# Kernel tuning notes

Hardware: AMD Instinct MI355X
Metric: run time of the kernel (lower is better)

## Reference

```python
import jax, jax.numpy as jnp
import numpy as np

B, IN_E, IN_I, D = 4096, 4096, 4096, 2048
IN_BR = 8192
BS = IN_BR // D  # block size = 4
K_E, K_I = 50, 1
E_TO_I = 50.0
BN_EPS = 1e-5


def setup_inputs() -> dict:
    key = jax.random.key(0)
    ks = jax.random.split(key, 8)
    # fan-in uniform init like nn.Linear (kaiming-uniform bound ~ 1/sqrt(in))
    def linw(k, out_f, in_f):
        b = 1.0 / np.sqrt(in_f)
        return jax.random.uniform(k, (out_f, in_f), jnp.float32, -b, b)
    return {
        "excitatory_input": jax.random.normal(ks[0], (B, IN_E), jnp.float32),
        "inhibitory_input": jax.random.normal(ks[1], (B, IN_I), jnp.float32),
        "dendrite_branch_outputs": jax.random.uniform(ks[2], (B, IN_BR), jnp.float32),
        "w_exc": linw(ks[3], D, IN_E),
        "w_inh": linw(ks[4], D, IN_I),
        "w_block": linw(ks[5], D, IN_BR),
        "bn_gamma": jnp.ones((D,), jnp.float32),
        "bn_beta": jnp.zeros((D,), jnp.float32),
    }


def _topk_linear(x, w, k):
    # keep the k largest weights per output row, zero the rest, then matmul
    idx = jax.lax.top_k(w, k)[1]                          # [D, k]
    mask = jnp.zeros_like(w).at[jnp.arange(w.shape[0])[:, None], idx].set(1.0)
    return x @ (w * mask).T                               # [B, D]


def _block_linear(x, w):
    # block-diagonal mask: row c uses columns [c*BS, (c+1)*BS)
    out_f = w.shape[0]
    wb = w.reshape(out_f, out_f, BS)[jnp.arange(out_f), jnp.arange(out_f)]  # [D, BS]
    xb = x.reshape(x.shape[0], out_f, BS)                                   # [B, D, BS]
    return jnp.einsum('bds,ds->bd', xb, wb)


def reference(excitatory_input, inhibitory_input, dendrite_branch_outputs,
              w_exc, w_inh, w_block, bn_gamma, bn_beta):
    dendrite_excitation = _topk_linear(excitatory_input, w_exc, K_E)
    dendrite_inhibition = _topk_linear(inhibitory_input, w_inh, K_I)
    dendrite_depolarization = _block_linear(dendrite_branch_outputs, w_block)
    total_excitatory = dendrite_excitation + dendrite_depolarization
    # neuron_type == 'excitatory'
    act = total_excitatory - E_TO_I * dendrite_inhibition
    # BatchNorm1d, training mode: batch stats, biased variance
    mean = jnp.mean(act, axis=0)
    var = jnp.var(act, axis=0)
    act = (act - mean) * jax.lax.rsqrt(var + BN_EPS) * bn_gamma + bn_beta
    return jax.nn.sigmoid(act)
```

## Files before the change

### kernel.cpp

```cpp
#include <hip/hip_runtime.h>
#include <hip/hip_fp16.h>

#define B_     4096
#define INE_   4096
#define INBR_  8192
#define D_     2048
#define KE_    50
#define KPAD_  52
#define CAP_   512
#define NSL_   4

__device__ __forceinline__ unsigned packh2(float a, float b) {
  __half2 h = __floats2half2_rn(a, b);
  return __builtin_bit_cast(unsigned, h);
}
__device__ __forceinline__ float2 unpackh2(unsigned u) {
  __half2 h = __builtin_bit_cast(__half2, u);
  return __half22float2(h);
}

__device__ void topk_body(const float* __restrict__ W, int row, int k, int kpad,
                          float hi, float t0, float vscale,
                          uint4* __restrict__ muT,
                          unsigned* __restrict__ out_off, float* __restrict__ out_val)
{
  const int t = threadIdx.x;
  const float* wr = W + (size_t)row * INE_;

  __shared__ float cval[CAP_];
  __shared__ int   ccol[CAP_];
  __shared__ int   scnt;
  __shared__ int   red[4];

  float thr = t0;
  int M = 0;
  for (int attempt = 0; attempt < 8; ++attempt) {
    int local = 0;
    #pragma unroll
    for (int j = 0; j < 4; ++j) {
      float4 w4 = *reinterpret_cast<const float4*>(wr + 4 * (t + 256 * j));
      local += (w4.x > thr) + (w4.y > thr) + (w4.z > thr) + (w4.w > thr);
    }
    #pragma unroll
    for (int off = 32; off > 0; off >>= 1) local += __shfl_down(local, off);
    if ((t & 63) == 0) red[t >> 6] = local;
    __syncthreads();
    M = red[0] + red[1] + red[2] + red[3];
    __syncthreads();
    if (M >= k && M <= CAP_) break;
    if (M < k) thr = hi - (hi - thr) * 4.0f;
    else       thr = hi - (hi - thr) * 0.5f;
  }

  if (t == 0) scnt = 0;
  __syncthreads();
  #pragma unroll
  for (int j = 0; j < 4; ++j) {
    int cbase = 4 * (t + 256 * j);
    float4 w4 = *reinterpret_cast<const float4*>(wr + cbase);
    float wv[4] = {w4.x, w4.y, w4.z, w4.w};
    #pragma unroll
    for (int q = 0; q < 4; ++q) {
      if (wv[q] > thr) {
        int pp = atomicAdd(&scnt, 1);
        if (pp < CAP_) { cval[pp] = wv[q]; ccol[pp] = cbase + q; }
      }
    }
  }
  __syncthreads();
  M = scnt < CAP_ ? scnt : CAP_;

  for (int i = t; i < M; i += 256) {
    float wi = cval[i]; int ci = ccol[i];
    int rank = 0;
    for (int m = 0; m < M; ++m) {
      float wm = cval[m]; int cm = ccol[m];
      rank += (wm > wi || (wm == wi && cm < ci)) ? 1 : 0;
    }
    if (rank < k) {
      unsigned c = (unsigned)ci;
      if (kpad == 1) {
        out_off[row] = c;
        out_val[row] = wi * vscale;
      } else {
        unsigned off = ((c >> 2) << 3) | ((c & 3u) << 13);
        char* rec = (char*)muT + ((size_t)(rank >> 2) * D_ + row) * 16;
        reinterpret_cast<unsigned short*>(rec)[rank & 3] = (unsigned short)off;
        reinterpret_cast<__half*>(rec)[4 + (rank & 3)] =
            __float2half_rn(wi * vscale);
      }
    }
  }
  if (kpad > 1 && t < kpad - k) {
    int slot = k + t;
    char* rec = (char*)muT + ((size_t)(slot >> 2) * D_ + row) * 16;
    reinterpret_cast<unsigned short*>(rec)[slot & 3] = 0;
    reinterpret_cast<__half*>(rec)[4 + (slot & 3)] = __float2half_rn(0.0f);
  }
}

__global__ __launch_bounds__(256) void prep_kernel(
    const float* __restrict__ wexc, const float* __restrict__ winh,
    const float* __restrict__ wblk,
    uint4* __restrict__ muT,
    unsigned* __restrict__ so_inh, float* __restrict__ vi_inh,
    float* __restrict__ wdiag)
{
  const int bid = blockIdx.x;
  const float hi = 0.015625f;
  if (bid < 2048) {
    topk_body(wexc, bid, KE_, KPAD_, hi, hi * (1.0f - 200.0f / 4096.0f), 1.0f,
              muT, nullptr, nullptr);
  } else if (bid < 4096) {
    topk_body(winh, bid - 2048, 1, 1, hi, hi * (1.0f - 48.0f / 4096.0f), -50.0f,
              nullptr, so_inh, vi_inh);
  } else {
    const int t = threadIdx.x;
    #pragma unroll
    for (int j = 0; j < 8; ++j) {
      int d = t + 256 * j;
      float4 w = *reinterpret_cast<const float4*>(wblk + (size_t)d * (INBR_ + 4));
      reinterpret_cast<float4*>(wdiag)[d] = w;
    }
  }
}

__device__ __forceinline__ uint2 ld8(const char* ldsb, unsigned off) {
  return *reinterpret_cast<const uint2*>(ldsb + off);
}

#define FMA4(R, G, WV) do {                                                \
    float2 f0 = unpackh2((G).x), f1 = unpackh2((G).y);                     \
    acc[R][0] = fmaf(f0.x, (WV), acc[R][0]);                               \
    acc[R][1] = fmaf(f0.y, (WV), acc[R][1]);                               \
    acc[R][2] = fmaf(f1.x, (WV), acc[R][2]);                               \
    acc[R][3] = fmaf(f1.y, (WV), acc[R][3]);                               \
  } while (0)

__global__ __launch_bounds__(512, 4) void fused_ei(
    const float* __restrict__ xe, const float* __restrict__ xi,
    const float* __restrict__ xbr, const float* __restrict__ wdiag,
    const uint4* __restrict__ muT,
    const unsigned* __restrict__ so_inh, const float* __restrict__ vi_inh,
    __half* __restrict__ act_h, float* __restrict__ sums_p,
    float* __restrict__ sumsq_p)
{
  __shared__ unsigned xs[8192];
  const int t  = threadIdx.x;
  const int b0 = blockIdx.x * 4;
  const int p  = t & 1;
  const int Q  = t >> 1;

  float acc[4][4];
  #pragma unroll
  for (int r = 0; r < 4; ++r)
    #pragma unroll
    for (int b = 0; b < 4; ++b) acc[r][b] = 0.0f;

  const char* ldsb = reinterpret_cast<const char*>(xs);

  {
    const float* r0p = xe + (size_t)(b0 + 2 * p)     * INE_;
    const float* r1p = xe + (size_t)(b0 + 2 * p + 1) * INE_;
    #pragma unroll
    for (int m = 0; m < 4; ++m) {
      int c0 = 4 * Q + 1024 * m;
      float4 fa = *reinterpret_cast<const float4*>(r0p + c0);
      float4 fb = *reinterpret_cast<const float4*>(r1p + c0);
      int wb = 2 * (Q + 256 * m) + p;
      xs[wb]        = packh2(fa.x, fb.x);
      xs[wb + 2048] = packh2(fa.y, fb.y);
      xs[wb + 4096] = packh2(fa.z, fb.z);
      xs[wb + 6144] = packh2(fa.w, fb.w);
    }
  }

  unsigned ci[4]; float viv[4];
  #pragma unroll
  for (int r = 0; r < 4; ++r) {
    ci[r]  = so_inh[t + 512 * r];
    viv[r] = vi_inh[t + 512 * r];
  }
  float xg0[4], xg1[4], xg2[4], xg3[4];
  #pragma unroll
  for (int b = 0; b < 4; ++b) {
    const float* xrow = xi + (size_t)(b0 + b) * INE_;
    xg0[b] = xrow[ci[0]];
    xg1[b] = xrow[ci[1]];
    xg2[b] = xrow[ci[2]];
    xg3[b] = xrow[ci[3]];
  }
  __syncthreads();

  for (int ii = 0; ii < KPAD_ / 4; ++ii) {
    uint4 m[4];
    #pragma unroll
    for (int r = 0; r < 4; ++r) m[r] = muT[ii * D_ + t + 512 * r];
    #pragma unroll
    for (int half = 0; half < 2; ++half) {
      uint2 g[2][4];
      #pragma unroll
      for (int rr = 0; rr < 2; ++rr) {
        const int r = 2 * half + rr;
        g[rr][0] = ld8(ldsb, m[r].x & 0xFFFFu);
        g[rr][1] = ld8(ldsb, m[r].x >> 16);
        g[rr][2] = ld8(ldsb, m[r].y & 0xFFFFu);
        g[rr][3] = ld8(ldsb, m[r].y >> 16);
      }
      #pragma unroll
      for (int rr = 0; rr < 2; ++rr) {
        const int r = 2 * half + rr;
        float2 vA = unpackh2(m[r].z);
        float2 vB = unpackh2(m[r].w);
        FMA4(r, g[rr][0], vA.x);
        FMA4(r, g[rr][1], vA.y);
        FMA4(r, g[rr][2], vB.x);
        FMA4(r, g[rr][3], vB.y);
      }
    }
  }

  #pragma unroll
  for (int b = 0; b < 4; ++b) {
    acc[0][b] = fmaf(xg0[b], viv[0], acc[0][b]);
    acc[1][b] = fmaf(xg1[b], viv[1], acc[1][b]);
    acc[2][b] = fmaf(xg2[b], viv[2], acc[2][b]);
    acc[3][b] = fmaf(xg3[b], viv[3], acc[3][b]);
  }

  #pragma unroll
  for (int r = 0; r < 4; ++r) {
    const int d = t + 512 * r;
    float4 wb4 = reinterpret_cast<const float4*>(wdiag)[d];
    #pragma unroll
    for (int b = 0; b < 4; ++b) {
      float4 xb4 = *reinterpret_cast<const float4*>(
          xbr + (size_t)(b0 + b) * INBR_ + 4 * d);
      acc[r][b] += xb4.x * wb4.x + xb4.y * wb4.y + xb4.z * wb4.z + xb4.w * wb4.w;
    }
  }

  const int slice = blockIdx.x & (NSL_ - 1);
  #pragma unroll
  for (int r = 0; r < 4; ++r) {
    const int d = t + 512 * r;
    float s = 0.0f, s2 = 0.0f;
    #pragma unroll
    for (int b = 0; b < 4; ++b) {
      float a = acc[r][b];
      act_h[(size_t)(b0 + b) * D_ + d] = __float2half_rn(a);
      s += a;
      s2 = fmaf(a, a, s2);
    }
    atomicAdd(&sums_p[slice * D_ + d], s);
    atomicAdd(&sumsq_p[slice * D_ + d], s2);
  }
}

__global__ __launch_bounds__(256) void tail_kernel(
    const __half* __restrict__ act_h, float* __restrict__ out,
    const float* __restrict__ sums_p, const float* __restrict__ sumsq_p,
    const float* __restrict__ gamma, const float* __restrict__ beta)
{
  __shared__ float scsh[2 * D_];
  const int tid = threadIdx.x;
  #pragma unroll
  for (int j = 0; j < 8; ++j) {
    int d = tid + 256 * j;
    float s = 0.0f, s2 = 0.0f;
    #pragma unroll
    for (int sl = 0; sl < NSL_; ++sl) {
      s  += sums_p[sl * D_ + d];
      s2 += sumsq_p[sl * D_ + d];
    }
    float mean = s  * (1.0f / B_);
    float var  = s2 * (1.0f / B_) - mean * mean;
    float rstd = rsqrtf(var + 1e-5f);
    float sc   = gamma[d] * rstd;
    scsh[2 * d]     = sc;
    scsh[2 * d + 1] = fmaf(-mean, sc, beta[d]);
  }
  __syncthreads();

  const int r0 = blockIdx.x * 8;
  for (int rr = 0; rr < 8; ++rr) {
    const uint2* ap = reinterpret_cast<const uint2*>(act_h + (size_t)(r0 + rr) * D_);
    float4*      op = reinterpret_cast<float4*>(out + (size_t)(r0 + rr) * D_);
    #pragma unroll
    for (int i2 = 0; i2 < 2; ++i2) {
      int i = tid + 256 * i2;
      uint2 aw = ap[i];
      float2 f0 = unpackh2(aw.x);
      float2 f1 = unpackh2(aw.y);
      const float4* sp = reinterpret_cast<const float4*>(scsh + 8 * i);
      float4 s0 = sp[0];
      float4 s1 = sp[1];
      float z0 = fmaf(f0.x, s0.x, s0.y);
      float z1 = fmaf(f0.y, s0.z, s0.w);
      float z2 = fmaf(f1.x, s1.x, s1.y);
      float z3 = fmaf(f1.y, s1.z, s1.w);
      float4 o;
      o.x = 1.0f / (1.0f + __expf(-z0));
      o.y = 1.0f / (1.0f + __expf(-z1));
      o.z = 1.0f / (1.0f + __expf(-z2));
      o.w = 1.0f / (1.0f + __expf(-z3));
      op[i] = o;
    }
  }
}

extern "C" void kernel_launch(void* const* d_in, const int* in_sizes, int n_in,
                              void* d_out, int out_size, void* d_ws, size_t ws_size,
                              hipStream_t stream) {
  const float* xe    = (const float*)d_in[0];
  const float* xi    = (const float*)d_in[1];
  const float* xbr   = (const float*)d_in[2];
  const float* wexc  = (const float*)d_in[3];
  const float* winh  = (const float*)d_in[4];
  const float* wblk  = (const float*)d_in[5];
  const float* gamma = (const float*)d_in[6];
  const float* beta  = (const float*)d_in[7];
  float* out = (float*)d_out;

  char* ws = (char*)d_ws;
  uint4*    muT     = (uint4*)   (ws + 0);
  unsigned* so_inh  = (unsigned*)(ws + 425984);
  float*    vi_inh  = (float*)   (ws + 434176);
  float*    wdiag   = (float*)   (ws + 442368);
  float*    sums_p  = (float*)   (ws + 475136);
  float*    sumsq_p = (float*)   (ws + 507904);
  __half*   act_h   = (__half*)  (ws + 1048576);

  hipMemsetAsync(sums_p, 0, 2 * NSL_ * D_ * sizeof(float), stream);

  prep_kernel<<<dim3(4097), dim3(256), 0, stream>>>(
      wexc, winh, wblk, muT, so_inh, vi_inh, wdiag);
  fused_ei<<<dim3(B_ / 4), dim3(512), 0, stream>>>(
      xe, xi, xbr, wdiag, muT, so_inh, vi_inh, act_h, sums_p, sumsq_p);
  tail_kernel<<<dim3(512), dim3(256), 0, stream>>>(
      act_h, out, sums_p, sumsq_p, gamma, beta);
}
```

Before: 124.6 us.

## Process two batch rows per block with 256 threads and 8 outputs each

Restructures the fused kernel so each block handles 2 batch rows instead of 4. It uses 256 threads, each owning 8 output columns, and halves the LDS tile to 16KB, so the packed offsets change to 4-byte gathers. The grid doubles, which needs more atomic slices, so NSL is raised to 8 and the workspace offset moves. The aim is higher occupancy and less LDS per block, at the cost of reading the muT index stream twice as many times (once per 2 rows instead of per 4).

```diff
diff --git a/kernel.cpp b/kernel.cpp
--- a/kernel.cpp
+++ b/kernel.cpp
@@ -8,7 +8,7 @@
 #define KE_    50
 #define KPAD_  52
 #define CAP_   512
-#define NSL_   4
+#define NSL_   8
 
 __device__ __forceinline__ unsigned packh2(float a, float b) {
   __half2 h = __floats2half2_rn(a, b);
@@ -83,7 +83,7 @@
         out_off[row] = c;
         out_val[row] = wi * vscale;
       } else {
-        unsigned off = ((c >> 2) << 3) | ((c & 3u) << 13);
+        unsigned off = ((c >> 2) << 2) | ((c & 3u) << 12);
         char* rec = (char*)muT + ((size_t)(rank >> 2) * D_ + row) * 16;
         reinterpret_cast<unsigned short*>(rec)[rank & 3] = (unsigned short)off;
         reinterpret_cast<__half*>(rec)[4 + (rank & 3)] =
@@ -125,19 +125,13 @@
   }
 }
 
-__device__ __forceinline__ uint2 ld8(const char* ldsb, unsigned off) {
-  return *reinterpret_cast<const uint2*>(ldsb + off);
-}
-
-#define FMA4(R, G, WV) do {                                                \
-    float2 f0 = unpackh2((G).x), f1 = unpackh2((G).y);                     \
-    acc[R][0] = fmaf(f0.x, (WV), acc[R][0]);                               \
-    acc[R][1] = fmaf(f0.y, (WV), acc[R][1]);                               \
-    acc[R][2] = fmaf(f1.x, (WV), acc[R][2]);                               \
-    acc[R][3] = fmaf(f1.y, (WV), acc[R][3]);                               \
+#define FMA2(R, W, WV) do {                                                \
+    float2 f = unpackh2(W);                                                \
+    acc[R][0] = fmaf(f.x, (WV), acc[R][0]);                                \
+    acc[R][1] = fmaf(f.y, (WV), acc[R][1]);                                \
   } while (0)
 
-__global__ __launch_bounds__(512, 4) void fused_ei(
+__global__ __launch_bounds__(256, 4) void fused_ei(
     const float* __restrict__ xe, const float* __restrict__ xi,
     const float* __restrict__ xbr, const float* __restrict__ wdiag,
     const uint4* __restrict__ muT,
@@ -145,115 +139,103 @@
     __half* __restrict__ act_h, float* __restrict__ sums_p,
     float* __restrict__ sumsq_p)
 {
-  __shared__ unsigned xs[8192];
+  __shared__ unsigned xs[4096];
   const int t  = threadIdx.x;
-  const int b0 = blockIdx.x * 4;
-  const int p  = t & 1;
-  const int Q  = t >> 1;
-
-  float acc[4][4];
+  const int b0 = blockIdx.x * 2;
+
+  float acc[8][2];
   #pragma unroll
-  for (int r = 0; r < 4; ++r)
-    #pragma unroll
-    for (int b = 0; b < 4; ++b) acc[r][b] = 0.0f;
+  for (int r = 0; r < 8; ++r) { acc[r][0] = 0.0f; acc[r][1] = 0.0f; }
 
   const char* ldsb = reinterpret_cast<const char*>(xs);
 
   {
-    const float* r0p = xe + (size_t)(b0 + 2 * p)     * INE_;
-    const float* r1p = xe + (size_t)(b0 + 2 * p + 1) * INE_;
+    const float* r0p = xe + (size_t)b0 * INE_;
+    const float* r1p = xe + (size_t)(b0 + 1) * INE_;
     #pragma unroll
     for (int m = 0; m < 4; ++m) {
-      int c0 = 4 * Q + 1024 * m;
+      int c0 = 4 * t + 1024 * m;
       float4 fa = *reinterpret_cast<const float4*>(r0p + c0);
       float4 fb = *reinterpret_cast<const float4*>(r1p + c0);
-      int wb = 2 * (Q + 256 * m) + p;
-      xs[wb]        = packh2(fa.x, fb.x);
-      xs[wb + 2048] = packh2(fa.y, fb.y);
-      xs[wb + 4096] = packh2(fa.z, fb.z);
-      xs[wb + 6144] = packh2(fa.w, fb.w);
-    }
-  }
-
-  unsigned ci[4]; float viv[4];
-  #pragma unroll
-  for (int r = 0; r < 4; ++r) {
-    ci[r]  = so_inh[t + 512 * r];
-    viv[r] = vi_inh[t + 512 * r];
-  }
-  float xg0[4], xg1[4], xg2[4], xg3[4];
-  #pragma unroll
-  for (int b = 0; b < 4; ++b) {
-    const float* xrow = xi + (size_t)(b0 + b) * INE_;
-    xg0[b] = xrow[ci[0]];
-    xg1[b] = xrow[ci[1]];
-    xg2[b] = xrow[ci[2]];
-    xg3[b] = xrow[ci[3]];
+      int w0 = t + 256 * m;
+      xs[w0]        = packh2(fa.x, fb.x);
+      xs[w0 + 1024] = packh2(fa.y, fb.y);
+      xs[w0 + 2048] = packh2(fa.z, fb.z);
+      xs[w0 + 3072] = packh2(fa.w, fb.w);
+    }
   }
   __syncthreads();
 
   for (int ii = 0; ii < KPAD_ / 4; ++ii) {
-    uint4 m[4];
-    #pragma unroll
-    for (int r = 0; r < 4; ++r) m[r] = muT[ii * D_ + t + 512 * r];
-    #pragma unroll
-    for (int half = 0; half < 2; ++half) {
-      uint2 g[2][4];
-      #pragma unroll
-      for (int rr = 0; rr < 2; ++rr) {
-        const int r = 2 * half + rr;
-        g[rr][0] = ld8(ldsb, m[r].x & 0xFFFFu);
-        g[rr][1] = ld8(ldsb, m[r].x >> 16);
-        g[rr][2] = ld8(ldsb, m[r].y & 0xFFFFu);
-        g[rr][3] = ld8(ldsb, m[r].y >> 16);
-      }
-      #pragma unroll
-      for (int rr = 0; rr < 2; ++rr) {
-        const int r = 2 * half + rr;
-        float2 vA = unpackh2(m[r].z);
-        float2 vB = unpackh2(m[r].w);
-        FMA4(r, g[rr][0], vA.x);
-        FMA4(r, g[rr][1], vA.y);
-        FMA4(r, g[rr][2], vB.x);
-        FMA4(r, g[rr][3], vB.y);
-      }
-    }
-  }
-
-  #pragma unroll
-  for (int b = 0; b < 4; ++b) {
-    acc[0][b] = fmaf(xg0[b], viv[0], acc[0][b]);
-    acc[1][b] = fmaf(xg1[b], viv[1], acc[1][b]);
-    acc[2][b] = fmaf(xg2[b], viv[2], acc[2][b]);
-    acc[3][b] = fmaf(xg3[b], viv[3], acc[3][b]);
-  }
-
-  #pragma unroll
-  for (int r = 0; r < 4; ++r) {
-    const int d = t + 512 * r;
-    float4 wb4 = reinterpret_cast<const float4*>(wdiag)[d];
-    #pragma unroll
-    for (int b = 0; b < 4; ++b) {
-      float4 xb4 = *reinterpret_cast<const float4*>(
-          xbr + (size_t)(b0 + b) * INBR_ + 4 * d);
-      acc[r][b] += xb4.x * wb4.x + xb4.y * wb4.y + xb4.z * wb4.z + xb4.w * wb4.w;
+    #pragma unroll
+    for (int rp = 0; rp < 4; ++rp) {
+      uint4 mA = muT[ii * D_ + t + 512 * rp];
+      uint4 mB = muT[ii * D_ + t + 512 * rp + 256];
+      unsigned gA0 = *reinterpret_cast<const unsigned*>(ldsb + (mA.x & 0xFFFFu));
+      unsigned gA1 = *reinterpret_cast<const unsigned*>(ldsb + (mA.x >> 16));
+      unsigned gA2 = *reinterpret_cast<const unsigned*>(ldsb + (mA.y & 0xFFFFu));
+      unsigned gA3 = *reinterpret_cast<const unsigned*>(ldsb + (mA.y >> 16));
+      unsigned gB0 = *reinterpret_cast<const unsigned*>(ldsb + (mB.x & 0xFFFFu));
+      unsigned gB1 = *reinterpret_cast<const unsigned*>(ldsb + (mB.x >> 16));
+      unsigned gB2 = *reinterpret_cast<const unsigned*>(ldsb + (mB.y & 0xFFFFu));
+      unsigned gB3 = *reinterpret_cast<const unsigned*>(ldsb + (mB.y >> 16));
+      const int rA = 2 * rp, rB = 2 * rp + 1;
+      float2 vA0 = unpackh2(mA.z), vA1 = unpackh2(mA.w);
+      float2 vB0 = unpackh2(mB.z), vB1 = unpackh2(mB.w);
+      FMA2(rA, gA0, vA0.x);
+      FMA2(rA, gA1, vA0.y);
+      FMA2(rA, gA2, vA1.x);
+      FMA2(rA, gA3, vA1.y);
+      FMA2(rB, gB0, vB0.x);
+      FMA2(rB, gB1, vB0.y);
+      FMA2(rB, gB2, vB1.x);
+      FMA2(rB, gB3, vB1.y);
+    }
+  }
+
+  {
+    const float* xr0 = xi + (size_t)b0 * INE_;
+    const float* xr1 = xi + (size_t)(b0 + 1) * INE_;
+    unsigned c[8]; float v[8];
+    #pragma unroll
+    for (int r = 0; r < 8; ++r) {
+      int d = t + 256 * r;
+      c[r] = so_inh[d];
+      v[r] = vi_inh[d];
+    }
+    float x0[8], x1[8];
+    #pragma unroll
+    for (int r = 0; r < 8; ++r) { x0[r] = xr0[c[r]]; x1[r] = xr1[c[r]]; }
+    #pragma unroll
+    for (int r = 0; r < 8; ++r) {
+      acc[r][0] = fmaf(x0[r], v[r], acc[r][0]);
+      acc[r][1] = fmaf(x1[r], v[r], acc[r][1]);
+    }
+  }
+
+  {
+    const float* xb0 = xbr + (size_t)b0 * INBR_;
+    const float* xb1 = xbr + (size_t)(b0 + 1) * INBR_;
+    #pragma unroll
+    for (int r = 0; r < 8; ++r) {
+      const int d = t + 256 * r;
+      float4 w4 = reinterpret_cast<const float4*>(wdiag)[d];
+      float4 x0 = *reinterpret_cast<const float4*>(xb0 + 4 * d);
+      float4 x1 = *reinterpret_cast<const float4*>(xb1 + 4 * d);
+      acc[r][0] += x0.x * w4.x + x0.y * w4.y + x0.z * w4.z + x0.w * w4.w;
+      acc[r][1] += x1.x * w4.x + x1.y * w4.y + x1.z * w4.z + x1.w * w4.w;
     }
   }
 
   const int slice = blockIdx.x & (NSL_ - 1);
   #pragma unroll
-  for (int r = 0; r < 4; ++r) {
-    const int d = t + 512 * r;
-    float s = 0.0f, s2 = 0.0f;
-    #pragma unroll
-    for (int b = 0; b < 4; ++b) {
-      float a = acc[r][b];
-      act_h[(size_t)(b0 + b) * D_ + d] = __float2half_rn(a);
-      s += a;
-      s2 = fmaf(a, a, s2);
-    }
-    atomicAdd(&sums_p[slice * D_ + d], s);
-    atomicAdd(&sumsq_p[slice * D_ + d], s2);
+  for (int r = 0; r < 8; ++r) {
+    const int d = t + 256 * r;
+    float a0 = acc[r][0], a1 = acc[r][1];
+    act_h[(size_t)b0 * D_ + d]       = __float2half_rn(a0);
+    act_h[(size_t)(b0 + 1) * D_ + d] = __float2half_rn(a1);
+    atomicAdd(&sums_p[slice * D_ + d], a0 + a1);
+    atomicAdd(&sumsq_p[slice * D_ + d], fmaf(a0, a0, a1 * a1));
   }
 }
 
@@ -328,14 +310,14 @@
   float*    vi_inh  = (float*)   (ws + 434176);
   float*    wdiag   = (float*)   (ws + 442368);
   float*    sums_p  = (float*)   (ws + 475136);
-  float*    sumsq_p = (float*)   (ws + 507904);
+  float*    sumsq_p = (float*)   (ws + 540672);
   __half*   act_h   = (__half*)  (ws + 1048576);
 
   hipMemsetAsync(sums_p, 0, 2 * NSL_ * D_ * sizeof(float), stream);
 
   prep_kernel<<<dim3(4097), dim3(256), 0, stream>>>(
       wexc, winh, wblk, muT, so_inh, vi_inh, wdiag);
-  fused_ei<<<dim3(B_ / 4), dim3(512), 0, stream>>>(
+  fused_ei<<<dim3(B_ / 2), dim3(256), 0, stream>>>(
       xe, xi, xbr, wdiag, muT, so_inh, vi_inh, act_h, sums_p, sumsq_p);
   tail_kernel<<<dim3(512), dim3(256), 0, stream>>>(
       act_h, out, sums_p, sumsq_p, gamma, beta);
```

After: 155.3 us. +24.6%, slower.

## Stage fp32 excitatory rows into LDS via direct global-to-LDS loads

Applied to the files above, without the earlier changes.

Replaces the register-staged fp16 pair-packed LDS tile with direct 16-byte global_load_lds copies of the four fp32 input rows, and changes the gather offsets and inner loop to fetch scalar floats per batch row. This removes the convert/pack work and the register round trip on staging, and keeps fp32 precision for the inputs. It also moves the inhibitory gather after the main loop to lower register pressure. In exchange, LDS use per block doubles to 64KB, which can cut resident blocks per CU, and each gather issues four LDS reads instead of one 8-byte read.

```diff
diff --git a/kernel.cpp b/kernel.cpp
--- a/kernel.cpp
+++ b/kernel.cpp
@@ -10,13 +10,15 @@
 #define CAP_   512
 #define NSL_   4
 
-__device__ __forceinline__ unsigned packh2(float a, float b) {
-  __half2 h = __floats2half2_rn(a, b);
-  return __builtin_bit_cast(unsigned, h);
-}
 __device__ __forceinline__ float2 unpackh2(unsigned u) {
   __half2 h = __builtin_bit_cast(__half2, u);
   return __half22float2(h);
+}
+
+__device__ __forceinline__ void gload_lds16(const float* g, float* l) {
+  __builtin_amdgcn_global_load_lds(
+      (const __attribute__((address_space(1))) void*)g,
+      (__attribute__((address_space(3))) void*)l, 16, 0, 0);
 }
 
 __device__ void topk_body(const float* __restrict__ W, int row, int k, int kpad,
@@ -83,9 +85,9 @@
         out_off[row] = c;
         out_val[row] = wi * vscale;
       } else {
-        unsigned off = ((c >> 2) << 3) | ((c & 3u) << 13);
         char* rec = (char*)muT + ((size_t)(rank >> 2) * D_ + row) * 16;
-        reinterpret_cast<unsigned short*>(rec)[rank & 3] = (unsigned short)off;
+        reinterpret_cast<unsigned short*>(rec)[rank & 3] =
+            (unsigned short)(c << 2);
         reinterpret_cast<__half*>(rec)[4 + (rank & 3)] =
             __float2half_rn(wi * vscale);
       }
@@ -125,17 +127,7 @@
   }
 }
 
-__device__ __forceinline__ uint2 ld8(const char* ldsb, unsigned off) {
-  return *reinterpret_cast<const uint2*>(ldsb + off);
-}
-
-#define FMA4(R, G, WV) do {                                                \
-    float2 f0 = unpackh2((G).x), f1 = unpackh2((G).y);                     \
-    acc[R][0] = fmaf(f0.x, (WV), acc[R][0]);                               \
-    acc[R][1] = fmaf(f0.y, (WV), acc[R][1]);                               \
-    acc[R][2] = fmaf(f1.x, (WV), acc[R][2]);                               \
-    acc[R][3] = fmaf(f1.y, (WV), acc[R][3]);                               \
-  } while (0)
+#define LDSF(OFF) (*reinterpret_cast<const float*>(ldsb + (OFF)))
 
 __global__ __launch_bounds__(512, 4) void fused_ei(
     const float* __restrict__ xe, const float* __restrict__ xi,
@@ -145,11 +137,9 @@
     __half* __restrict__ act_h, float* __restrict__ sums_p,
     float* __restrict__ sumsq_p)
 {
-  __shared__ unsigned xs[8192];
+  __shared__ float xs_f[16384];
   const int t  = threadIdx.x;
   const int b0 = blockIdx.x * 4;
-  const int p  = t & 1;
-  const int Q  = t >> 1;
 
   float acc[4][4];
   #pragma unroll
@@ -157,38 +147,19 @@
     #pragma unroll
     for (int b = 0; b < 4; ++b) acc[r][b] = 0.0f;
 
-  const char* ldsb = reinterpret_cast<const char*>(xs);
+  const char* ldsb = reinterpret_cast<const char*>(xs_f);
 
   {
-    const float* r0p = xe + (size_t)(b0 + 2 * p)     * INE_;
-    const float* r1p = xe + (size_t)(b0 + 2 * p + 1) * INE_;
-    #pragma unroll
-    for (int m = 0; m < 4; ++m) {
-      int c0 = 4 * Q + 1024 * m;
-      float4 fa = *reinterpret_cast<const float4*>(r0p + c0);
-      float4 fb = *reinterpret_cast<const float4*>(r1p + c0);
-      int wb = 2 * (Q + 256 * m) + p;
-      xs[wb]        = packh2(fa.x, fb.x);
-      xs[wb + 2048] = packh2(fa.y, fb.y);
-      xs[wb + 4096] = packh2(fa.z, fb.z);
-      xs[wb + 6144] = packh2(fa.w, fb.w);
-    }
-  }
-
-  unsigned ci[4]; float viv[4];
-  #pragma unroll
-  for (int r = 0; r < 4; ++r) {
-    ci[r]  = so_inh[t + 512 * r];
-    viv[r] = vi_inh[t + 512 * r];
-  }
-  float xg0[4], xg1[4], xg2[4], xg3[4];
-  #pragma unroll
-  for (int b = 0; b < 4; ++b) {
-    const float* xrow = xi + (size_t)(b0 + b) * INE_;
-    xg0[b] = xrow[ci[0]];
-    xg1[b] = xrow[ci[1]];
-    xg2[b] = xrow[ci[2]];
-    xg3[b] = xrow[ci[3]];
+    const int wave = t >> 6, lane = t & 63;
+    #pragma unroll
+    for (int j = 0; j < 8; ++j) {
+      int k   = wave * 8 + j;
+      int row = k >> 4;
+      int cin = (k & 15) << 8;
+      const float* g = xe + (size_t)(b0 + row) * INE_ + cin + lane * 4;
+      float*       l = xs_f + row * 4096 + cin + lane * 4;
+      gload_lds16(g, l);
+    }
   }
   __syncthreads();
 
@@ -197,35 +168,62 @@
     #pragma unroll
     for (int r = 0; r < 4; ++r) m[r] = muT[ii * D_ + t + 512 * r];
     #pragma unroll
-    for (int half = 0; half < 2; ++half) {
-      uint2 g[2][4];
-      #pragma unroll
-      for (int rr = 0; rr < 2; ++rr) {
-        const int r = 2 * half + rr;
-        g[rr][0] = ld8(ldsb, m[r].x & 0xFFFFu);
-        g[rr][1] = ld8(ldsb, m[r].x >> 16);
-        g[rr][2] = ld8(ldsb, m[r].y & 0xFFFFu);
-        g[rr][3] = ld8(ldsb, m[r].y >> 16);
-      }
-      #pragma unroll
-      for (int rr = 0; rr < 2; ++rr) {
-        const int r = 2 * half + rr;
-        float2 vA = unpackh2(m[r].z);
-        float2 vB = unpackh2(m[r].w);
-        FMA4(r, g[rr][0], vA.x);
-        FMA4(r, g[rr][1], vA.y);
-        FMA4(r, g[rr][2], vB.x);
-        FMA4(r, g[rr][3], vB.y);
-      }
-    }
-  }
-
-  #pragma unroll
-  for (int b = 0; b < 4; ++b) {
-    acc[0][b] = fmaf(xg0[b], viv[0], acc[0][b]);
-    acc[1][b] = fmaf(xg1[b], viv[1], acc[1][b]);
-    acc[2][b] = fmaf(xg2[b], viv[2], acc[2][b]);
-    acc[3][b] = fmaf(xg3[b], viv[3], acc[3][b]);
+    for (int r = 0; r < 4; ++r) {
+      unsigned o0 = m[r].x & 0xFFFFu, o1 = m[r].x >> 16;
+      unsigned o2 = m[r].y & 0xFFFFu, o3 = m[r].y >> 16;
+      float2 vA = unpackh2(m[r].z);
+      float2 vB = unpackh2(m[r].w);
+      float g00 = LDSF(o0), g01 = LDSF(o0 + 16384),
+            g02 = LDSF(o0 + 32768), g03 = LDSF(o0 + 49152);
+      float g10 = LDSF(o1), g11 = LDSF(o1 + 16384),
+            g12 = LDSF(o1 + 32768), g13 = LDSF(o1 + 49152);
+      float g20 = LDSF(o2), g21 = LDSF(o2 + 16384),
+            g22 = LDSF(o2 + 32768), g23 = LDSF(o2 + 49152);
+      float g30 = LDSF(o3), g31 = LDSF(o3 + 16384),
+            g32 = LDSF(o3 + 32768), g33 = LDSF(o3 + 49152);
+      acc[r][0] = fmaf(g00, vA.x, acc[r][0]);
+      acc[r][1] = fmaf(g01, vA.x, acc[r][1]);
+      acc[r][2] = fmaf(g02, vA.x, acc[r][2]);
+      acc[r][3] = fmaf(g03, vA.x, acc[r][3]);
+      acc[r][0] = fmaf(g10, vA.y, acc[r][0]);
+      acc[r][1] = fmaf(g11, vA.y, acc[r][1]);
+      acc[r][2] = fmaf(g12, vA.y, acc[r][2]);
+      acc[r][3] = fmaf(g13, vA.y, acc[r][3]);
+      acc[r][0] = fmaf(g20, vB.x, acc[r][0]);
+      acc[r][1] = fmaf(g21, vB.x, acc[r][1]);
+      acc[r][2] = fmaf(g22, vB.x, acc[r][2]);
+      acc[r][3] = fmaf(g23, vB.x, acc[r][3]);
+      acc[r][0] = fmaf(g30, vB.y, acc[r][0]);
+      acc[r][1] = fmaf(g31, vB.y, acc[r][1]);
+      acc[r][2] = fmaf(g32, vB.y, acc[r][2]);
+      acc[r][3] = fmaf(g33, vB.y, acc[r][3]);
+    }
+  }
+
+
+  {
+    unsigned ci[4]; float viv[4];
+    #pragma unroll
+    for (int r = 0; r < 4; ++r) {
+      ci[r]  = so_inh[t + 512 * r];
+      viv[r] = vi_inh[t + 512 * r];
+    }
+    float xg0[4], xg1[4], xg2[4], xg3[4];
+    #pragma unroll
+    for (int b = 0; b < 4; ++b) {
+      const float* xrow = xi + (size_t)(b0 + b) * INE_;
+      xg0[b] = xrow[ci[0]];
+      xg1[b] = xrow[ci[1]];
+      xg2[b] = xrow[ci[2]];
+      xg3[b] = xrow[ci[3]];
+    }
+    #pragma unroll
+    for (int b = 0; b < 4; ++b) {
+      acc[0][b] = fmaf(xg0[b], viv[0], acc[0][b]);
+      acc[1][b] = fmaf(xg1[b], viv[1], acc[1][b]);
+      acc[2][b] = fmaf(xg2[b], viv[2], acc[2][b]);
+      acc[3][b] = fmaf(xg3[b], viv[3], acc[3][b]);
+    }
   }
 
   #pragma unroll
```

Measured after the change: 162.6 us. 30.5% more time.
